# Optimization experiments

Measured on AMD Instinct MI355X. Metric: run time of the kernel, lower is better.

Reference implementation:

```python
import jax, jax.numpy as jnp
import numpy as np

N_NODES = 50000
N_EDGES = 800000
VOCAB = 1000
EMBED = 64
HIDDEN = 64
N_CLASSES = 10
N_GRAPHS = 512


def setup_inputs() -> dict:
    key = jax.random.key(0)
    ks = jax.random.split(key, 10)
    tokens = jax.random.randint(ks[0], (N_NODES,), 0, VOCAB)
    edge_index = jax.random.randint(ks[1], (2, N_EDGES), 0, N_NODES)
    batch = jnp.sort(jax.random.randint(ks[2], (N_NODES,), 0, N_GRAPHS))
    emb = jax.random.normal(ks[3], (VOCAB, EMBED), jnp.float32) * 0.02
    emb = emb.at[0].set(0.0)  # padding_idx=0
    W1 = jax.random.normal(ks[4], (EMBED, HIDDEN), jnp.float32) * (1.0 / np.sqrt(EMBED))
    b1 = jnp.zeros((HIDDEN,), jnp.float32)
    W2 = jax.random.normal(ks[5], (HIDDEN, HIDDEN), jnp.float32) * (1.0 / np.sqrt(HIDDEN))
    b2 = jnp.zeros((HIDDEN,), jnp.float32)
    lin_W = jax.random.normal(ks[6], (HIDDEN, N_CLASSES), jnp.float32) * (1.0 / np.sqrt(HIDDEN))
    lin_b = jnp.zeros((N_CLASSES,), jnp.float32)
    return {"tokens": tokens, "edge_index": edge_index, "batch": batch,
            "emb": emb, "W1": W1, "b1": b1, "W2": W2, "b2": b2,
            "lin_W": lin_W, "lin_b": lin_b}


def _gcn_conv(x, src, dst, W, b, n_nodes):
    # PyG GCNConv: add self-loops, symmetric normalization D^-1/2 (A+I) D^-1/2
    ones = jnp.ones((src.shape[0],), x.dtype)
    deg = jax.ops.segment_sum(ones, dst, num_segments=n_nodes) + 1.0  # self-loop
    dis = jnp.where(deg > 0, jax.lax.rsqrt(deg), 0.0)
    h = x @ W  # linear first (no bias)
    coef = dis[src] * dis[dst]                      # [E]
    msg = h[src] * coef[:, None]                    # gather + scale
    agg = jax.ops.segment_sum(msg, dst, num_segments=n_nodes)
    agg = agg + h * (dis * dis)[:, None]            # self-loop message
    return agg + b


def reference(tokens, edge_index, batch, emb, W1, b1, W2, b2, lin_W, lin_b):
    src, dst = edge_index[0], edge_index[1]
    x = emb[tokens]                                  # [N, EMBED]
    x = jax.nn.relu(_gcn_conv(x, src, dst, W1, b1, N_NODES))
    x = jax.nn.relu(_gcn_conv(x, src, dst, W2, b2, N_NODES))
    # global_mean_pool over batch ids
    sums = jax.ops.segment_sum(x, batch, num_segments=N_GRAPHS)
    cnts = jax.ops.segment_sum(jnp.ones((x.shape[0],), x.dtype), batch, num_segments=N_GRAPHS)
    pooled = sums / jnp.maximum(cnts, 1.0)[:, None]  # [G, HIDDEN]
    return pooled @ lin_W + lin_b
```

## Files before the change

### kernel.cpp

```cpp
#include <hip/hip_runtime.h>

#define NGRAPHS 512
#define D 64
#define NCLS 10
#define TILE 256

__global__ void k_deg(const int* __restrict__ dst, int* __restrict__ degi,
                      int* __restrict__ rank, int E) {
  int i = blockIdx.x * blockDim.x + threadIdx.x;
  if (i < E) rank[i] = atomicAdd(&degi[dst[i]], 1);
}

__global__ __launch_bounds__(TILE) void k_part(const int* __restrict__ degi,
                                               int* __restrict__ bsum, int n) {
  __shared__ int red[TILE];
  int t = threadIdx.x;
  int i = blockIdx.x * TILE + t;
  red[t] = (i < n) ? degi[i] : 0;
  __syncthreads();
  for (int off = TILE / 2; off > 0; off >>= 1) {
    if (t < off) red[t] += red[t + off];
    __syncthreads();
  }
  if (t == 0) bsum[blockIdx.x] = red[0];
}

__global__ __launch_bounds__(TILE) void k_scanb(const int* __restrict__ bsum,
                                                int* __restrict__ boff, int nb) {
  __shared__ int s[TILE];
  int t = threadIdx.x;
  s[t] = (t < nb) ? bsum[t] : 0;
  __syncthreads();
  for (int off = 1; off < TILE; off <<= 1) {
    int v = (t >= off) ? s[t - off] : 0;
    __syncthreads();
    s[t] += v;
    __syncthreads();
  }
  if (t < nb) boff[t] = (t > 0) ? s[t - 1] : 0;
}

__global__ __launch_bounds__(TILE) void k_emit(const int* __restrict__ degi,
                                               const int* __restrict__ boff,
                                               int* __restrict__ rowstart,
                                               float* __restrict__ dis, int n) {
  __shared__ int s[TILE];
  int t = threadIdx.x;
  int i = blockIdx.x * TILE + t;
  int v = (i < n) ? degi[i] : 0;
  s[t] = v;
  __syncthreads();
  for (int off = 1; off < TILE; off <<= 1) {
    int u = (t >= off) ? s[t - off] : 0;
    __syncthreads();
    s[t] += u;
    __syncthreads();
  }
  if (i < n) {
    int incl = s[t] + boff[blockIdx.x];
    rowstart[i] = incl - v;
    dis[i] = rsqrtf((float)v + 1.0f);
    if (i == n - 1) rowstart[n] = incl;
  }
}

__global__ void k_fill(const int* __restrict__ src, const int* __restrict__ dst,
                       const int* __restrict__ rank, const int* __restrict__ rowstart,
                       int* __restrict__ eci, int E) {
  int e = blockIdx.x * blockDim.x + threadIdx.x;
  if (e < E) {
    eci[rowstart[dst[e]] + rank[e]] = src[e];
  }
}

__global__ __launch_bounds__(256) void k_agg1e(const float4* __restrict__ emb4,
                                               const int* __restrict__ tokens,
                                               const int* __restrict__ eci,
                                               const int* __restrict__ rowstart,
                                               const float* __restrict__ dis,
                                               float4* __restrict__ out, int n) {
  int tid = blockIdx.x * blockDim.x + threadIdx.x;
  int node = tid >> 6;
  int lane = tid & 63;
  int slot = lane >> 4;
  int cg = lane & 15;
  if (node >= n) return;
  int beg = rowstart[node], end = rowstart[node + 1];
  float4 acc = make_float4(0.f, 0.f, 0.f, 0.f);
  int j = beg + slot;
  for (; j + 12 < end; j += 16) {
    int s0 = eci[j], s1 = eci[j + 4], s2 = eci[j + 8], s3 = eci[j + 12];
    int t0 = tokens[s0], t1 = tokens[s1], t2 = tokens[s2], t3 = tokens[s3];
    float w0 = dis[s0], w1 = dis[s1], w2 = dis[s2], w3 = dis[s3];
    float4 v0 = emb4[(size_t)t0 * 16 + cg];
    float4 v1 = emb4[(size_t)t1 * 16 + cg];
    float4 v2 = emb4[(size_t)t2 * 16 + cg];
    float4 v3 = emb4[(size_t)t3 * 16 + cg];
    acc.x += w0 * v0.x + w1 * v1.x + w2 * v2.x + w3 * v3.x;
    acc.y += w0 * v0.y + w1 * v1.y + w2 * v2.y + w3 * v3.y;
    acc.z += w0 * v0.z + w1 * v1.z + w2 * v2.z + w3 * v3.z;
    acc.w += w0 * v0.w + w1 * v1.w + w2 * v2.w + w3 * v3.w;
  }
  for (; j < end; j += 4) {
    int s = eci[j];
    float w = dis[s];
    float4 v = emb4[(size_t)tokens[s] * 16 + cg];
    acc.x += w * v.x; acc.y += w * v.y; acc.z += w * v.z; acc.w += w * v.w;
  }
  acc.x += __shfl_xor(acc.x, 16, 64); acc.y += __shfl_xor(acc.y, 16, 64);
  acc.z += __shfl_xor(acc.z, 16, 64); acc.w += __shfl_xor(acc.w, 16, 64);
  acc.x += __shfl_xor(acc.x, 32, 64); acc.y += __shfl_xor(acc.y, 32, 64);
  acc.z += __shfl_xor(acc.z, 32, 64); acc.w += __shfl_xor(acc.w, 32, 64);
  if (slot == 0) {
    float wd = dis[node];
    float4 vd = emb4[(size_t)tokens[node] * 16 + cg];
    acc.x = wd * (acc.x + wd * vd.x);
    acc.y = wd * (acc.y + wd * vd.y);
    acc.z = wd * (acc.z + wd * vd.z);
    acc.w = wd * (acc.w + wd * vd.w);
    out[(size_t)node * 16 + cg] = acc;
  }
}

template <bool SCALE>
__global__ __launch_bounds__(256) void k_gemmrelu(const float* __restrict__ x,
                                                  const float* __restrict__ W,
                                                  const float* __restrict__ bias,
                                                  const float* __restrict__ dis,
                                                  float4* __restrict__ o4, int n) {
  __shared__ float Ws[64 * 64];
  int tid = threadIdx.x;
  for (int i = tid; i < 64 * 64; i += 256) Ws[i] = W[i];
  __syncthreads();
  const float4* Ws4 = (const float4*)Ws;
  int w = tid >> 6, lane = tid & 63;
  int cg = lane & 15;
  int kb = lane & 48;
  for (int node = blockIdx.x * 4 + w; node < n; node += gridDim.x * 4) {
    float xval = x[(size_t)node * D + lane];
    float4 acc = make_float4(0.f, 0.f, 0.f, 0.f);
#pragma unroll
    for (int p = 0; p < 16; ++p) {
      float xv = __shfl(xval, kb + p, 64);
      float4 wv = Ws4[(kb + p) * 16 + cg];
      acc.x += xv * wv.x; acc.y += xv * wv.y;
      acc.z += xv * wv.z; acc.w += xv * wv.w;
    }
    acc.x += __shfl_xor(acc.x, 16, 64); acc.y += __shfl_xor(acc.y, 16, 64);
    acc.z += __shfl_xor(acc.z, 16, 64); acc.w += __shfl_xor(acc.w, 16, 64);
    acc.x += __shfl_xor(acc.x, 32, 64); acc.y += __shfl_xor(acc.y, 32, 64);
    acc.z += __shfl_xor(acc.z, 32, 64); acc.w += __shfl_xor(acc.w, 32, 64);
    if (lane < 16) {
      float4 bv = ((const float4*)bias)[cg];
      float4 r;
      r.x = fmaxf(acc.x + bv.x, 0.f);
      r.y = fmaxf(acc.y + bv.y, 0.f);
      r.z = fmaxf(acc.z + bv.z, 0.f);
      r.w = fmaxf(acc.w + bv.w, 0.f);
      if (SCALE) {
        float dd = dis[node];
        r.x *= dd; r.y *= dd; r.z *= dd; r.w *= dd;
      }
      o4[(size_t)node * 16 + cg] = r;
    }
  }
}

__global__ __launch_bounds__(256) void k_aggs(const float4* __restrict__ h4,
                                              const int* __restrict__ eci,
                                              const int* __restrict__ rowstart,
                                              const float* __restrict__ dis,
                                              float4* __restrict__ out, int n) {
  int tid = blockIdx.x * blockDim.x + threadIdx.x;
  int node = tid >> 6;
  int lane = tid & 63;
  int slot = lane >> 4;
  int cg = lane & 15;
  if (node >= n) return;
  int beg = rowstart[node], end = rowstart[node + 1];
  float4 acc = make_float4(0.f, 0.f, 0.f, 0.f);
  int i = beg + slot;
  for (; i + 12 < end; i += 16) {
    int s0 = eci[i], s1 = eci[i + 4], s2 = eci[i + 8], s3 = eci[i + 12];
    float4 v0 = h4[(size_t)s0 * 16 + cg];
    float4 v1 = h4[(size_t)s1 * 16 + cg];
    float4 v2 = h4[(size_t)s2 * 16 + cg];
    float4 v3 = h4[(size_t)s3 * 16 + cg];
    acc.x += (v0.x + v1.x) + (v2.x + v3.x);
    acc.y += (v0.y + v1.y) + (v2.y + v3.y);
    acc.z += (v0.z + v1.z) + (v2.z + v3.z);
    acc.w += (v0.w + v1.w) + (v2.w + v3.w);
  }
  for (; i < end; i += 4) {
    float4 v = h4[(size_t)eci[i] * 16 + cg];
    acc.x += v.x; acc.y += v.y; acc.z += v.z; acc.w += v.w;
  }
  acc.x += __shfl_xor(acc.x, 16, 64); acc.y += __shfl_xor(acc.y, 16, 64);
  acc.z += __shfl_xor(acc.z, 16, 64); acc.w += __shfl_xor(acc.w, 16, 64);
  acc.x += __shfl_xor(acc.x, 32, 64); acc.y += __shfl_xor(acc.y, 32, 64);
  acc.z += __shfl_xor(acc.z, 32, 64); acc.w += __shfl_xor(acc.w, 32, 64);
  if (slot == 0) {
    float dd = dis[node];
    float4 hv = h4[(size_t)node * 16 + cg];
    acc.x = dd * (acc.x + hv.x);
    acc.y = dd * (acc.y + hv.y);
    acc.z = dd * (acc.z + hv.z);
    acc.w = dd * (acc.w + hv.w);
    out[(size_t)node * 16 + cg] = acc;
  }
}

__device__ __forceinline__ int lower_bound(const int* __restrict__ a, int n, int v) {
  int lo = 0, hi = n;
  while (lo < hi) {
    int m = (lo + hi) >> 1;
    if (a[m] < v) lo = m + 1; else hi = m;
  }
  return lo;
}

__global__ __launch_bounds__(256) void k_poolfinal(const float* __restrict__ x,
                                                   const int* __restrict__ batch,
                                                   const float* __restrict__ lw,
                                                   const float* __restrict__ lb,
                                                   float* __restrict__ out, int n) {
  __shared__ float red[4][64];
  __shared__ float pooled[64];
  int g = blockIdx.x;
  int s = lower_bound(batch, n, g);
  int e = lower_bound(batch, n, g + 1);
  int w = threadIdx.x >> 6, lane = threadIdx.x & 63;
  float acc = 0.f;
  for (int i = s + w; i < e; i += 4) acc += x[(size_t)i * D + lane];
  red[w][lane] = acc;
  __syncthreads();
  if (w == 0) {
    float v = red[0][lane] + red[1][lane] + red[2][lane] + red[3][lane];
    pooled[lane] = v / fmaxf((float)(e - s), 1.0f);
  }
  __syncthreads();
  if (threadIdx.x < NCLS) {
    int c = threadIdx.x;
    float a = lb[c];
#pragma unroll
    for (int k = 0; k < D; ++k) a += pooled[k] * lw[k * NCLS + c];
    out[g * NCLS + c] = a;
  }
}

extern "C" void kernel_launch(void* const* d_in, const int* in_sizes, int n_in,
                              void* d_out, int out_size, void* d_ws, size_t ws_size,
                              hipStream_t stream) {
  const int* tokens = (const int*)d_in[0];
  const int* edge   = (const int*)d_in[1];
  const int* batch  = (const int*)d_in[2];
  const float* emb  = (const float*)d_in[3];
  const float* W1   = (const float*)d_in[4];
  const float* b1   = (const float*)d_in[5];
  const float* W2   = (const float*)d_in[6];
  const float* b2   = (const float*)d_in[7];
  const float* lw   = (const float*)d_in[8];
  const float* lb   = (const float*)d_in[9];
  float* out = (float*)d_out;

  const int N = in_sizes[0];
  const int E = in_sizes[1] / 2;
  const int* src  = edge;
  const int* dstv = edge + E;

  const int nb = (N + TILE - 1) / TILE;

  char* ws = (char*)d_ws;
  size_t off = 0;
  auto alloc = [&](size_t bytes) {
    void* p = ws + off;
    off += (bytes + 255) & ~(size_t)255;
    return p;
  };
  float* A        = (float*)alloc((size_t)N * D * sizeof(float));
  float* B        = (float*)alloc((size_t)N * D * sizeof(float));
  int*   eci      = (int*)alloc((size_t)E * sizeof(int));
  int*   rank     = (int*)alloc((size_t)E * sizeof(int));
  float* dis      = (float*)alloc((size_t)N * sizeof(float));
  int*   degi     = (int*)alloc((size_t)N * sizeof(int));
  int*   rowstart = (int*)alloc(((size_t)N + 1) * sizeof(int));
  int*   bsum     = (int*)alloc((size_t)nb * sizeof(int));
  int*   boff     = (int*)alloc((size_t)nb * sizeof(int));

  hipMemsetAsync(degi, 0, (size_t)N * sizeof(int), stream);

  k_deg<<<(E + 255) / 256, 256, 0, stream>>>(dstv, degi, rank, E);
  k_part<<<nb, TILE, 0, stream>>>(degi, bsum, N);
  k_scanb<<<1, TILE, 0, stream>>>(bsum, boff, nb);
  k_emit<<<nb, TILE, 0, stream>>>(degi, boff, rowstart, dis, N);
  k_fill<<<(E + 255) / 256, 256, 0, stream>>>(src, dstv, rank, rowstart, eci, E);

  const int nodeBlocks = (N + 3) / 4;
  const int gemmGrid = 2048;

  k_agg1e<<<nodeBlocks, 256, 0, stream>>>((const float4*)emb, tokens, eci, rowstart,
                                          dis, (float4*)A, N);
  k_gemmrelu<true><<<gemmGrid, 256, 0, stream>>>(A, W1, b1, dis, (float4*)B, N);
  k_aggs<<<nodeBlocks, 256, 0, stream>>>((const float4*)B, eci, rowstart, dis,
                                         (float4*)A, N);
  k_gemmrelu<false><<<gemmGrid, 256, 0, stream>>>(A, W2, b2, nullptr, (float4*)B, N);
  k_poolfinal<<<NGRAPHS, 256, 0, stream>>>(B, batch, lw, lb, out, N);
}
```

Before: 185.1 us.

## Precompute emb@W1 per token and drop one node-level GEMM pass

Layer 1 now multiplies the 1000-row embedding table by W1 once, inside the same launch as the CSR fill, rather than running a GEMM over all 50k aggregated nodes. The aggregation then gathers pre-transformed rows and applies bias, ReLU and the dis scaling in its epilogue. The CSR stores (src, token) pairs so the token lookup no longer needs a dependent load. Layer 2 now runs the GEMM before aggregation, with bias and ReLU fused into the aggregation, which removes a full N×64 GEMM pass and one round trip of intermediate data at the cost of a wider edge array.

```diff
diff --git a/kernel.cpp b/kernel.cpp
--- a/kernel.cpp
+++ b/kernel.cpp
@@ -64,20 +64,53 @@
   }
 }
 
-__global__ void k_fill(const int* __restrict__ src, const int* __restrict__ dst,
-                       const int* __restrict__ rank, const int* __restrict__ rowstart,
-                       int* __restrict__ eci, int E) {
-  int e = blockIdx.x * blockDim.x + threadIdx.x;
-  if (e < E) {
-    eci[rowstart[dst[e]] + rank[e]] = src[e];
-  }
-}
-
-__global__ __launch_bounds__(256) void k_agg1e(const float4* __restrict__ emb4,
+__global__ __launch_bounds__(256) void k_filltok(
+    const int* __restrict__ src, const int* __restrict__ dst,
+    const int* __restrict__ rank, const int* __restrict__ rowstart,
+    const int* __restrict__ tokens, int2* __restrict__ ec2, int E,
+    const float* __restrict__ emb, const float* __restrict__ W1,
+    float4* __restrict__ ht4, int ntok, int fillBlocks, int tokBlocks) {
+  if (blockIdx.x < fillBlocks) {
+    int e = blockIdx.x * 256 + threadIdx.x;
+    if (e < E) {
+      int s = src[e];
+      ec2[rowstart[dst[e]] + rank[e]] = make_int2(s, tokens[s]);
+    }
+    return;
+  }
+  __shared__ float Ws[64 * 64];
+  int tid = threadIdx.x;
+  for (int i = tid; i < 64 * 64; i += 256) Ws[i] = W1[i];
+  __syncthreads();
+  const float4* Ws4 = (const float4*)Ws;
+  int w = tid >> 6, lane = tid & 63;
+  int cg = lane & 15;
+  int kb = lane & 48;
+  int bid = blockIdx.x - fillBlocks;
+  for (int tok = bid * 4 + w; tok < ntok; tok += tokBlocks * 4) {
+    float xval = emb[(size_t)tok * D + lane];
+    float4 acc = make_float4(0.f, 0.f, 0.f, 0.f);
+#pragma unroll
+    for (int p = 0; p < 16; ++p) {
+      float xv = __shfl(xval, kb + p, 64);
+      float4 wv = Ws4[(kb + p) * 16 + cg];
+      acc.x += xv * wv.x; acc.y += xv * wv.y;
+      acc.z += xv * wv.z; acc.w += xv * wv.w;
+    }
+    acc.x += __shfl_xor(acc.x, 16, 64); acc.y += __shfl_xor(acc.y, 16, 64);
+    acc.z += __shfl_xor(acc.z, 16, 64); acc.w += __shfl_xor(acc.w, 16, 64);
+    acc.x += __shfl_xor(acc.x, 32, 64); acc.y += __shfl_xor(acc.y, 32, 64);
+    acc.z += __shfl_xor(acc.z, 32, 64); acc.w += __shfl_xor(acc.w, 32, 64);
+    if (lane < 16) ht4[(size_t)tok * 16 + cg] = acc;
+  }
+}
+
+__global__ __launch_bounds__(256) void k_agg1t(const float4* __restrict__ ht4,
+                                               const int2* __restrict__ ec2,
+                                               const int* __restrict__ rowstart,
                                                const int* __restrict__ tokens,
-                                               const int* __restrict__ eci,
-                                               const int* __restrict__ rowstart,
                                                const float* __restrict__ dis,
+                                               const float4* __restrict__ b14,
                                                float4* __restrict__ out, int n) {
   int tid = blockIdx.x * blockDim.x + threadIdx.x;
   int node = tid >> 6;
@@ -89,22 +122,21 @@
   float4 acc = make_float4(0.f, 0.f, 0.f, 0.f);
   int j = beg + slot;
   for (; j + 12 < end; j += 16) {
-    int s0 = eci[j], s1 = eci[j + 4], s2 = eci[j + 8], s3 = eci[j + 12];
-    int t0 = tokens[s0], t1 = tokens[s1], t2 = tokens[s2], t3 = tokens[s3];
-    float w0 = dis[s0], w1 = dis[s1], w2 = dis[s2], w3 = dis[s3];
-    float4 v0 = emb4[(size_t)t0 * 16 + cg];
-    float4 v1 = emb4[(size_t)t1 * 16 + cg];
-    float4 v2 = emb4[(size_t)t2 * 16 + cg];
-    float4 v3 = emb4[(size_t)t3 * 16 + cg];
+    int2 e0 = ec2[j], e1 = ec2[j + 4], e2 = ec2[j + 8], e3 = ec2[j + 12];
+    float w0 = dis[e0.x], w1 = dis[e1.x], w2 = dis[e2.x], w3 = dis[e3.x];
+    float4 v0 = ht4[(size_t)e0.y * 16 + cg];
+    float4 v1 = ht4[(size_t)e1.y * 16 + cg];
+    float4 v2 = ht4[(size_t)e2.y * 16 + cg];
+    float4 v3 = ht4[(size_t)e3.y * 16 + cg];
     acc.x += w0 * v0.x + w1 * v1.x + w2 * v2.x + w3 * v3.x;
     acc.y += w0 * v0.y + w1 * v1.y + w2 * v2.y + w3 * v3.y;
     acc.z += w0 * v0.z + w1 * v1.z + w2 * v2.z + w3 * v3.z;
     acc.w += w0 * v0.w + w1 * v1.w + w2 * v2.w + w3 * v3.w;
   }
   for (; j < end; j += 4) {
-    int s = eci[j];
-    float w = dis[s];
-    float4 v = emb4[(size_t)tokens[s] * 16 + cg];
+    int2 e = ec2[j];
+    float w = dis[e.x];
+    float4 v = ht4[(size_t)e.y * 16 + cg];
     acc.x += w * v.x; acc.y += w * v.y; acc.z += w * v.z; acc.w += w * v.w;
   }
   acc.x += __shfl_xor(acc.x, 16, 64); acc.y += __shfl_xor(acc.y, 16, 64);
@@ -112,22 +144,21 @@
   acc.x += __shfl_xor(acc.x, 32, 64); acc.y += __shfl_xor(acc.y, 32, 64);
   acc.z += __shfl_xor(acc.z, 32, 64); acc.w += __shfl_xor(acc.w, 32, 64);
   if (slot == 0) {
-    float wd = dis[node];
-    float4 vd = emb4[(size_t)tokens[node] * 16 + cg];
-    acc.x = wd * (acc.x + wd * vd.x);
-    acc.y = wd * (acc.y + wd * vd.y);
-    acc.z = wd * (acc.z + wd * vd.z);
-    acc.w = wd * (acc.w + wd * vd.w);
-    out[(size_t)node * 16 + cg] = acc;
-  }
-}
-
-template <bool SCALE>
-__global__ __launch_bounds__(256) void k_gemmrelu(const float* __restrict__ x,
-                                                  const float* __restrict__ W,
-                                                  const float* __restrict__ bias,
-                                                  const float* __restrict__ dis,
-                                                  float4* __restrict__ o4, int n) {
+    float dd = dis[node];
+    float4 vd = ht4[(size_t)tokens[node] * 16 + cg];
+    float4 bv = b14[cg];
+    float4 r;
+    r.x = dd * fmaxf(dd * (acc.x + dd * vd.x) + bv.x, 0.f);
+    r.y = dd * fmaxf(dd * (acc.y + dd * vd.y) + bv.y, 0.f);
+    r.z = dd * fmaxf(dd * (acc.z + dd * vd.z) + bv.z, 0.f);
+    r.w = dd * fmaxf(dd * (acc.w + dd * vd.w) + bv.w, 0.f);
+    out[(size_t)node * 16 + cg] = r;
+  }
+}
+
+__global__ __launch_bounds__(256) void k_gemmp(const float* __restrict__ x,
+                                               const float* __restrict__ W,
+                                               float4* __restrict__ o4, int n) {
   __shared__ float Ws[64 * 64];
   int tid = threadIdx.x;
   for (int i = tid; i < 64 * 64; i += 256) Ws[i] = W[i];
@@ -150,26 +181,15 @@
     acc.z += __shfl_xor(acc.z, 16, 64); acc.w += __shfl_xor(acc.w, 16, 64);
     acc.x += __shfl_xor(acc.x, 32, 64); acc.y += __shfl_xor(acc.y, 32, 64);
     acc.z += __shfl_xor(acc.z, 32, 64); acc.w += __shfl_xor(acc.w, 32, 64);
-    if (lane < 16) {
-      float4 bv = ((const float4*)bias)[cg];
-      float4 r;
-      r.x = fmaxf(acc.x + bv.x, 0.f);
-      r.y = fmaxf(acc.y + bv.y, 0.f);
-      r.z = fmaxf(acc.z + bv.z, 0.f);
-      r.w = fmaxf(acc.w + bv.w, 0.f);
-      if (SCALE) {
-        float dd = dis[node];
-        r.x *= dd; r.y *= dd; r.z *= dd; r.w *= dd;
-      }
-      o4[(size_t)node * 16 + cg] = r;
-    }
+    if (lane < 16) o4[(size_t)node * 16 + cg] = acc;
   }
 }
 
 __global__ __launch_bounds__(256) void k_aggs(const float4* __restrict__ h4,
-                                              const int* __restrict__ eci,
+                                              const int2* __restrict__ ec2,
                                               const int* __restrict__ rowstart,
                                               const float* __restrict__ dis,
+                                              const float4* __restrict__ b24,
                                               float4* __restrict__ out, int n) {
   int tid = blockIdx.x * blockDim.x + threadIdx.x;
   int node = tid >> 6;
@@ -181,7 +201,7 @@
   float4 acc = make_float4(0.f, 0.f, 0.f, 0.f);
   int i = beg + slot;
   for (; i + 12 < end; i += 16) {
-    int s0 = eci[i], s1 = eci[i + 4], s2 = eci[i + 8], s3 = eci[i + 12];
+    int s0 = ec2[i].x, s1 = ec2[i + 4].x, s2 = ec2[i + 8].x, s3 = ec2[i + 12].x;
     float4 v0 = h4[(size_t)s0 * 16 + cg];
     float4 v1 = h4[(size_t)s1 * 16 + cg];
     float4 v2 = h4[(size_t)s2 * 16 + cg];
@@ -192,7 +212,7 @@
     acc.w += (v0.w + v1.w) + (v2.w + v3.w);
   }
   for (; i < end; i += 4) {
-    float4 v = h4[(size_t)eci[i] * 16 + cg];
+    float4 v = h4[(size_t)ec2[i].x * 16 + cg];
     acc.x += v.x; acc.y += v.y; acc.z += v.z; acc.w += v.w;
   }
   acc.x += __shfl_xor(acc.x, 16, 64); acc.y += __shfl_xor(acc.y, 16, 64);
@@ -202,10 +222,11 @@
   if (slot == 0) {
     float dd = dis[node];
     float4 hv = h4[(size_t)node * 16 + cg];
-    acc.x = dd * (acc.x + hv.x);
-    acc.y = dd * (acc.y + hv.y);
-    acc.z = dd * (acc.z + hv.z);
-    acc.w = dd * (acc.w + hv.w);
+    float4 bv = b24[cg];
+    acc.x = fmaxf(dd * (acc.x + hv.x) + bv.x, 0.f);
+    acc.y = fmaxf(dd * (acc.y + hv.y) + bv.y, 0.f);
+    acc.z = fmaxf(dd * (acc.z + hv.z) + bv.z, 0.f);
+    acc.w = fmaxf(dd * (acc.w + hv.w) + bv.w, 0.f);
     out[(size_t)node * 16 + cg] = acc;
   }
 }
@@ -265,6 +286,7 @@
 
   const int N = in_sizes[0];
   const int E = in_sizes[1] / 2;
+  const int ntok = in_sizes[3] / D;
   const int* src  = edge;
   const int* dstv = edge + E;
 
@@ -279,11 +301,12 @@
   };
   float* A        = (float*)alloc((size_t)N * D * sizeof(float));
   float* B        = (float*)alloc((size_t)N * D * sizeof(float));
-  int*   eci      = (int*)alloc((size_t)E * sizeof(int));
+  int2*  ec2      = (int2*)alloc((size_t)E * sizeof(int2));
   int*   rank     = (int*)alloc((size_t)E * sizeof(int));
   float* dis      = (float*)alloc((size_t)N * sizeof(float));
   int*   degi     = (int*)alloc((size_t)N * sizeof(int));
   int*   rowstart = (int*)alloc(((size_t)N + 1) * sizeof(int));
+  float* ht       = (float*)alloc((size_t)ntok * D * sizeof(float));
   int*   bsum     = (int*)alloc((size_t)nb * sizeof(int));
   int*   boff     = (int*)alloc((size_t)nb * sizeof(int));
 
@@ -293,16 +316,20 @@
   k_part<<<nb, TILE, 0, stream>>>(degi, bsum, N);
   k_scanb<<<1, TILE, 0, stream>>>(bsum, boff, nb);
   k_emit<<<nb, TILE, 0, stream>>>(degi, boff, rowstart, dis, N);
-  k_fill<<<(E + 255) / 256, 256, 0, stream>>>(src, dstv, rank, rowstart, eci, E);
+
+  const int fillBlocks = (E + 255) / 256;
+  const int tokBlocks = (ntok + 3) / 4;
+  k_filltok<<<fillBlocks + tokBlocks, 256, 0, stream>>>(
+      src, dstv, rank, rowstart, tokens, ec2, E, emb, W1, (float4*)ht, ntok,
+      fillBlocks, tokBlocks);
 
   const int nodeBlocks = (N + 3) / 4;
   const int gemmGrid = 2048;
 
-  k_agg1e<<<nodeBlocks, 256, 0, stream>>>((const float4*)emb, tokens, eci, rowstart,
-                                          dis, (float4*)A, N);
-  k_gemmrelu<true><<<gemmGrid, 256, 0, stream>>>(A, W1, b1, dis, (float4*)B, N);
-  k_aggs<<<nodeBlocks, 256, 0, stream>>>((const float4*)B, eci, rowstart, dis,
-                                         (float4*)A, N);
-  k_gemmrelu<false><<<gemmGrid, 256, 0, stream>>>(A, W2, b2, nullptr, (float4*)B, N);
+  k_agg1t<<<nodeBlocks, 256, 0, stream>>>((const float4*)ht, ec2, rowstart, tokens,
+                                          dis, (const float4*)b1, (float4*)B, N);
+  k_gemmp<<<gemmGrid, 256, 0, stream>>>(B, W2, (float4*)A, N);
+  k_aggs<<<nodeBlocks, 256, 0, stream>>>((const float4*)A, ec2, rowstart, dis,
+                                         (const float4*)b2, (float4*)B, N);
   k_poolfinal<<<NGRAPHS, 256, 0, stream>>>(B, batch, lw, lb, out, N);
 }
```

Result: faster. 166.7 us (-10.0%).
